# Kernel tuning notes

Measured on AMD Instinct MI355X. Metric: run time of the kernel, lower is better.

## Reference

```python
import jax, jax.numpy as jnp
import numpy as np
from jax import lax

# TT-conv configuration (matches init_kwargs)
M = (4, 8, 8)        # in_c_modes, prod = 256
O = (4, 8, 8)        # out_c_modes, prod = 256
R = (16, 16, 16, 1)  # ranks with trailing 1 appended as in the module
B, H, W = 8, 64, 64
IN_C = int(np.prod(M))


def setup_inputs() -> dict:
    key = jax.random.key(0)
    ks = jax.random.split(key, 6)
    X = jax.random.normal(ks[0], (B, IN_C, H, W), jnp.float32)
    conv_w = jax.random.normal(ks[1], (R[0], 1, 3, 3), jnp.float32) * 0.3
    conv_b = jax.random.normal(ks[2], (R[0],), jnp.float32) * 0.05
    def xavier(k, shape):
        fan_in, fan_out = shape[1], shape[0]
        std = (2.0 / (fan_in + fan_out)) ** 0.5
        return jax.random.normal(k, shape, jnp.float32) * std
    core1 = xavier(ks[3], (O[0] * R[1], R[0] * M[0]))  # (64, 64)
    core2 = xavier(ks[4], (O[1] * R[2], R[1] * M[1]))  # (128, 128)
    core3 = xavier(ks[5], (O[2] * R[3], R[2] * M[2]))  # (8, 128)
    return {"X": X, "conv_w": conv_w, "conv_b": conv_b,
            "core1": core1, "core2": core2, "core3": core3}


def reference(X, conv_w, conv_b, core1, core2, core3):
    b, in_c, h, w = X.shape
    # core0: depth-agnostic 1->r0 conv applied per input channel
    y = lax.conv_general_dilated(
        X.reshape(-1, 1, h, w), conv_w,
        window_strides=(1, 1), padding=((1, 1), (1, 1)),
        dimension_numbers=("NCHW", "OIHW", "NCHW"))
    y = y + conv_b[None, :, None, None]          # (B*in_c, r0, h, w)
    hh, ww = y.shape[-2:]
    # (B, m1, m2, m3, r0, h, w): in_c factored row-major, m1 most significant
    y = y.reshape(b, M[0], M[1], M[2], R[0], hh, ww)
    # TT cores reshaped (o_i, r_{i+1}, r_i, m_i)
    G1 = core1.reshape(O[0], R[1], R[0], M[0])
    G2 = core2.reshape(O[1], R[2], R[1], M[1])
    G3 = core3.reshape(O[2], R[3], R[2], M[2])
    # Full TT contraction chain collapsed into one einsum; s (=r3) has size 1.
    out = jnp.einsum("bijkrhw,auri,cvuj,dsvk->bacdhw",
                     y, G1, G2, G3, optimize=True)
    # channel order (o1, o2, o3) with o3 fastest, as in the torch module
    return out.reshape(b, O[0] * O[1] * O[2], hh, ww)
```

## Files before the change

kernel.cpp:

```cpp
#include <hip/hip_runtime.h>
#include <hip/hip_bf16.h>
#include <stdint.h>

typedef __attribute__((ext_vector_type(8))) short short8;
typedef __attribute__((ext_vector_type(4))) float f32x4;

#define XP_BYTES   17842176
#define XP_PAD     1024
#define OFF_W9     (XP_BYTES + XP_PAD)
#define W9_BYTES   (8*9*4*256*8*2)
#define OFF_BIAS   (OFF_W9 + W9_BYTES)

__device__ __forceinline__ short f2bf(float f) {
  __hip_bfloat16 h = __float2bfloat16(f);
  return *reinterpret_cast<short*>(&h);
}

__device__ __forceinline__ void gl_lds16(const void* g, void* l) {
  __builtin_amdgcn_global_load_lds(
      (const __attribute__((address_space(1))) void*)g,
      (__attribute__((address_space(3))) void*)l, 16, 0, 0);
}

__global__ void k_prep(const float* __restrict__ X,
                       const float* __restrict__ core1,
                       const float* __restrict__ core2,
                       const float* __restrict__ core3,
                       const float* __restrict__ convw,
                       const float* __restrict__ convb,
                       short* __restrict__ Xp, short* __restrict__ W9,
                       float* __restrict__ bias) {
  __shared__ float H2s[1024];
  __shared__ float red[256];

  if (blockIdx.z == 8) {
    if (blockIdx.y >= 4) return;
    const int o = blockIdx.y * 64 + blockIdx.x;
    const int c = threadIdx.x;
    const int a = o >> 6, c2 = (o >> 3) & 7, d = o & 7;
#pragma unroll
    for (int p = 0; p < 4; ++p) {
      int idx = c + (p << 8);
      int k = idx & 7, j = (idx >> 3) & 7, u = idx >> 6;
      float s = 0.f;
#pragma unroll
      for (int v = 0; v < 16; ++v)
        s += core2[(c2 * 16 + v) * 128 + u * 8 + j] * core3[d * 128 + v * 8 + k];
      H2s[idx] = s;
    }
    __syncthreads();
    const int i = c >> 6, j = (c >> 3) & 7, k = c & 7;
    float Wr[16];
#pragma unroll
    for (int r = 0; r < 16; ++r) Wr[r] = 0.f;
    for (int u = 0; u < 16; ++u) {
      float h = H2s[u * 64 + j * 8 + k];
      const float* c1 = core1 + (a * 16 + u) * 64 + i;
#pragma unroll
      for (int r = 0; r < 16; ++r) Wr[r] += c1[r * 4] * h;
    }
    const int cb = c >> 5, cl = c & 31, g = cl >> 3, pos = cl & 7;
#pragma unroll
    for (int t = 0; t < 9; ++t) {
      float s = 0.f;
#pragma unroll
      for (int r = 0; r < 16; ++r) s += Wr[r] * convw[r * 9 + t];
      W9[(((size_t)(((cb * 9 + t) << 2) + g) << 8) + o) * 8 + pos] = f2bf(s);
    }
    float s = 0.f;
#pragma unroll
    for (int r = 0; r < 16; ++r) s += Wr[r] * convb[r];
    red[c] = s;
    __syncthreads();
    for (int st = 128; st > 0; st >>= 1) {
      if (c < st) red[c] += red[c + st];
      __syncthreads();
    }
    if (c == 0) bias[o] = red[0];
    return;
  }

  const int y = blockIdx.x, b = blockIdx.y, cb = blockIdx.z;
  const int t = threadIdx.x;
  short8* XpG = (short8*)Xp;
  const size_t slice = (size_t)(b * 8 + cb) * 66 * 4 * 66;
  const short8 z8 = {0, 0, 0, 0, 0, 0, 0, 0};
  if (t < 8) {
    const int xg = (t >> 2) ? 65 : 0;
    XpG[slice + ((size_t)(y + 1) * 4 + (t & 3)) * 66 + xg] = z8;
  }
  if (y == 0)
    for (int g = t; g < 264; g += 256) XpG[slice + g] = z8;
  if (y == 63)
    for (int g = t; g < 264; g += 256) XpG[slice + (size_t)65 * 264 + g] = z8;
  const int x = t & 63, sub = t >> 6;
  const float* src = X + ((size_t)(b * 256 + cb * 32 + sub * 8) * 64 + y) * 64 + x;
  short8 v;
#pragma unroll
  for (int k = 0; k < 8; ++k) v[k] = f2bf(src[(size_t)k * 4096]);
  XpG[slice + ((size_t)(y + 1) * 4 + sub) * 66 + (x + 1)] = v;
}

__global__ __launch_bounds__(256, 2) void k_gemm(
    const short* __restrict__ Xp, const short* __restrict__ W9,
    const float* __restrict__ bias, float* __restrict__ out) {
  __shared__ __align__(16) short XL[12800];
  __shared__ __align__(16) short WL[18720];

  const int tid  = threadIdx.x;
  const int lane = tid & 63;
  const int wv   = tid >> 6;
  const int l15  = lane & 15;
  const int gl   = lane >> 4;
  const int h0    = blockIdx.x << 2;
  const int oBase = blockIdx.y << 6;
  const int b     = blockIdx.z;

  f32x4 acc[4][4];
#pragma unroll
  for (int io = 0; io < 4; ++io)
#pragma unroll
    for (int ip = 0; ip < 4; ++ip)
      acc[io][ip] = (f32x4){0.f, 0.f, 0.f, 0.f};

  for (int cb = 0; cb < 8; ++cb) {
    __syncthreads();
#pragma unroll 1
    for (int q = wv; q < 36; q += 4) {
      const short* g = W9 + (((((size_t)(cb * 36 + q)) << 8) + oBase + lane) << 3);
      gl_lds16(g, &WL[(q * 65 + lane) << 3]);
    }
    const size_t xbG = ((size_t)(((b << 3) + cb) * 66 + h0)) * 264;
#pragma unroll 1
    for (int q = wv; q < 25; q += 4) {
      gl_lds16(Xp + ((xbG + (q << 6) + lane) << 3), &XL[(q << 9) + (lane << 3)]);
    }
    __syncthreads();
#pragma unroll
    for (int t = 0; t < 9; ++t) {
      const int dy = t / 3, dx = t % 3;
      const int row = wv + dy;
      short8 af[4], bfr[4];
#pragma unroll
      for (int io = 0; io < 4; ++io) {
        const int ol = (io << 4) + l15;
        af[io] = *(const short8*)&WL[((((t << 2) + gl) * 65) + ol) << 3];
      }
#pragma unroll
      for (int ip = 0; ip < 4; ++ip) {
        const int x = (ip << 4) + l15 + dx;
        bfr[ip] = *(const short8*)&XL[((((row << 2) + gl) * 66) + x) << 3];
      }
#pragma unroll
      for (int io = 0; io < 4; ++io)
#pragma unroll
        for (int ip = 0; ip < 4; ++ip)
          acc[io][ip] = __builtin_amdgcn_mfma_f32_16x16x32_bf16(
              af[io], bfr[ip], acc[io][ip], 0, 0, 0);
    }
  }

  const int h = h0 + wv;
#pragma unroll
  for (int io = 0; io < 4; ++io) {
#pragma unroll
    for (int r = 0; r < 4; ++r) {
      const int oG = oBase + (io << 4) + (gl << 2) + r;
      const float bv = bias[oG];
      float* op = out + (((size_t)((b << 8) + oG)) << 12) + (h << 6);
#pragma unroll
      for (int ip = 0; ip < 4; ++ip)
        op[(ip << 4) + l15] = acc[io][ip][r] + bv;
    }
  }
}

extern "C" void kernel_launch(void* const* d_in, const int* in_sizes, int n_in,
                              void* d_out, int out_size, void* d_ws, size_t ws_size,
                              hipStream_t stream) {
  (void)in_sizes; (void)n_in; (void)out_size; (void)ws_size;
  const float* X     = (const float*)d_in[0];
  const float* convw = (const float*)d_in[1];
  const float* convb = (const float*)d_in[2];
  const float* core1 = (const float*)d_in[3];
  const float* core2 = (const float*)d_in[4];
  const float* core3 = (const float*)d_in[5];
  float* out = (float*)d_out;
  char*  ws  = (char*)d_ws;

  short* Xp   = (short*)ws;
  short* W9   = (short*)(ws + OFF_W9);
  float* bias = (float*)(ws + OFF_BIAS);

  k_prep<<<dim3(64, 8, 9), 256, 0, stream>>>(X, core1, core2, core3, convw,
                                             convb, Xp, W9, bias);
  k_gemm<<<dim3(16, 4, 8), 256, 0, stream>>>(Xp, W9, bias, out);
}
```

Before: 145.1 us.

## Double output rows per block and split weight taps into two LDS phases

Each block now computes 8 output rows instead of 4, with each wave handling two rows and 32 accumulator tiles. This doubles weight reuse per LDS load and halves the grid to 256 blocks. To fit the larger input tile in LDS, the 9 weight taps are staged in two batches (5 then 4) with extra barriers. Occupancy drops to one block per CU, and the extra syncs serialize loads with compute.

After: 156.2 us. +7.6%, slower.

```diff
diff --git a/kernel.cpp b/kernel.cpp
--- a/kernel.cpp
+++ b/kernel.cpp
@@ -101,76 +101,89 @@
   XpG[slice + ((size_t)(y + 1) * 4 + sub) * 66 + (x + 1)] = v;
 }
 
-__global__ __launch_bounds__(256, 2) void k_gemm(
+template <int T0, int NT>
+__device__ __forceinline__ void do_taps(const short* XLp, const short* WLp,
+                                        int wv, int l15, int gl,
+                                        f32x4 (&acc)[4][8]) {
+#pragma unroll
+  for (int tl = 0; tl < NT; ++tl) {
+    const int t = T0 + tl;
+    const int dy = t / 3, dx = t % 3;
+    short8 af[4], bfr[8];
+#pragma unroll
+    for (int io = 0; io < 4; ++io)
+      af[io] = *(const short8*)&WLp[(((((tl << 2) + gl) << 6) + (io << 4) + l15)) << 3];
+#pragma unroll
+    for (int ip = 0; ip < 8; ++ip) {
+      const int rowL = (wv << 1) + dy + (ip >> 2);
+      const int x = ((ip & 3) << 4) + l15 + dx;
+      bfr[ip] = *(const short8*)&XLp[((((rowL << 2) + gl) * 66) + x) << 3];
+    }
+#pragma unroll
+    for (int io = 0; io < 4; ++io)
+#pragma unroll
+      for (int ip = 0; ip < 8; ++ip)
+        acc[io][ip] = __builtin_amdgcn_mfma_f32_16x16x32_bf16(
+            af[io], bfr[ip], acc[io][ip], 0, 0, 0);
+  }
+}
+
+__global__ __launch_bounds__(256, 1) void k_gemm(
     const short* __restrict__ Xp, const short* __restrict__ W9,
     const float* __restrict__ bias, float* __restrict__ out) {
-  __shared__ __align__(16) short XL[12800];
-  __shared__ __align__(16) short WL[18720];
+  __shared__ __align__(16) short XL[21504];
+  __shared__ __align__(16) short WL[10240];
 
   const int tid  = threadIdx.x;
   const int lane = tid & 63;
   const int wv   = tid >> 6;
   const int l15  = lane & 15;
   const int gl   = lane >> 4;
-  const int h0    = blockIdx.x << 2;
+  const int h0    = blockIdx.x << 3;
   const int oBase = blockIdx.y << 6;
   const int b     = blockIdx.z;
 
-  f32x4 acc[4][4];
+  f32x4 acc[4][8];
 #pragma unroll
   for (int io = 0; io < 4; ++io)
 #pragma unroll
-    for (int ip = 0; ip < 4; ++ip)
+    for (int ip = 0; ip < 8; ++ip)
       acc[io][ip] = (f32x4){0.f, 0.f, 0.f, 0.f};
 
   for (int cb = 0; cb < 8; ++cb) {
     __syncthreads();
-#pragma unroll 1
-    for (int q = wv; q < 36; q += 4) {
-      const short* g = W9 + (((((size_t)(cb * 36 + q)) << 8) + oBase + lane) << 3);
-      gl_lds16(g, &WL[(q * 65 + lane) << 3]);
-    }
     const size_t xbG = ((size_t)(((b << 3) + cb) * 66 + h0)) * 264;
 #pragma unroll 1
-    for (int q = wv; q < 25; q += 4) {
-      gl_lds16(Xp + ((xbG + (q << 6) + lane) << 3), &XL[(q << 9) + (lane << 3)]);
-    }
-    __syncthreads();
-#pragma unroll
-    for (int t = 0; t < 9; ++t) {
-      const int dy = t / 3, dx = t % 3;
-      const int row = wv + dy;
-      short8 af[4], bfr[4];
-#pragma unroll
-      for (int io = 0; io < 4; ++io) {
-        const int ol = (io << 4) + l15;
-        af[io] = *(const short8*)&WL[((((t << 2) + gl) * 65) + ol) << 3];
-      }
-#pragma unroll
-      for (int ip = 0; ip < 4; ++ip) {
-        const int x = (ip << 4) + l15 + dx;
-        bfr[ip] = *(const short8*)&XL[((((row << 2) + gl) * 66) + x) << 3];
-      }
-#pragma unroll
-      for (int io = 0; io < 4; ++io)
-#pragma unroll
-        for (int ip = 0; ip < 4; ++ip)
-          acc[io][ip] = __builtin_amdgcn_mfma_f32_16x16x32_bf16(
-              af[io], bfr[ip], acc[io][ip], 0, 0, 0);
-    }
-  }
-
-  const int h = h0 + wv;
+    for (int q = wv; q < 42; q += 4)
+      gl_lds16(Xp + ((xbG + (q << 6) + lane) << 3), &XL[((q << 6) + lane) << 3]);
+#pragma unroll 1
+    for (int q = wv; q < 20; q += 4)
+      gl_lds16(W9 + ((((size_t)(cb * 36 + q) << 8) + oBase + lane) << 3),
+               &WL[((q << 6) + lane) << 3]);
+    __syncthreads();
+    do_taps<0, 5>(XL, WL, wv, l15, gl, acc);
+    __syncthreads();
+#pragma unroll 1
+    for (int q = wv; q < 16; q += 4)
+      gl_lds16(W9 + ((((size_t)(cb * 36 + 20 + q) << 8) + oBase + lane) << 3),
+               &WL[((q << 6) + lane) << 3]);
+    __syncthreads();
+    do_taps<5, 4>(XL, WL, wv, l15, gl, acc);
+  }
+
+  const int hA = h0 + (wv << 1);
 #pragma unroll
   for (int io = 0; io < 4; ++io) {
 #pragma unroll
     for (int r = 0; r < 4; ++r) {
       const int oG = oBase + (io << 4) + (gl << 2) + r;
       const float bv = bias[oG];
-      float* op = out + (((size_t)((b << 8) + oG)) << 12) + (h << 6);
-#pragma unroll
-      for (int ip = 0; ip < 4; ++ip)
-        op[(ip << 4) + l15] = acc[io][ip][r] + bv;
+      float* op = out + (((size_t)((b << 8) + oG)) << 12);
+#pragma unroll
+      for (int ip = 0; ip < 8; ++ip) {
+        const int h = hA + (ip >> 2);
+        op[(h << 6) + ((ip & 3) << 4) + l15] = acc[io][ip][r] + bv;
+      }
     }
   }
 }
@@ -194,5 +207,5 @@
 
   k_prep<<<dim3(64, 8, 9), 256, 0, stream>>>(X, core1, core2, core3, convw,
                                              convb, Xp, W9, bias);
-  k_gemm<<<dim3(16, 4, 8), 256, 0, stream>>>(Xp, W9, bias, out);
-}
+  k_gemm<<<dim3(8, 4, 8), 256, 0, stream>>>(Xp, W9, bias, out);
+}
```
